# Optimization experiments

Measured on AMD Instinct MI355X. Metric: run time of the kernel, lower is better.

The kernel has to match this reference:

```python
import jax, jax.numpy as jnp
import numpy as np

B, M, T, D, V = 16, 4096, 4, 256, 40000
HOPS, NLAYER, CONV_MAX = 3, 3, 512
PAD = 1  # PAD_token: embedding row zeroed (padding_idx)


def setup_inputs() -> dict:
    key = jax.random.key(0)
    ks = jax.random.split(key, 10)
    story = jax.random.randint(ks[0], (B, M, T), 0, V)
    conv_len = jax.random.randint(ks[1], (B,), 1, CONV_MAX)
    kb_len = jax.random.randint(ks[2], (B,), 0, M - CONV_MAX)
    query = jax.random.normal(ks[3], (B, 1, D), jnp.float32)
    history_outputs = jax.random.normal(ks[4], (B, CONV_MAX, D), jnp.float32)
    query_vector = jax.random.normal(ks[5], (B, D), jnp.float32)
    global_pointer = jax.random.uniform(ks[6], (B, M), jnp.float32)
    # hop+1 embedding tables, N(0, 0.1), padding row zeroed
    C_emb = jax.random.normal(ks[7], (HOPS + 1, V, D), jnp.float32) * 0.1
    C_emb = C_emb.at[:, PAD, :].set(0.0)
    Tg_w = jax.random.normal(ks[8], (HOPS + 1, D, D), jnp.float32) * 0.05
    Tg_b = jnp.zeros((HOPS + 1, D), jnp.float32)
    FW_w = jax.random.normal(ks[9], (D, D), jnp.float32) * 0.05
    FW_b = jnp.zeros((D,), jnp.float32)
    return dict(story=story, kb_len=kb_len, conv_len=conv_len, query=query,
                history_outputs=history_outputs, query_vector=query_vector,
                global_pointer=global_pointer, C_emb=C_emb, Tg_w=Tg_w,
                Tg_b=Tg_b, FW_w=FW_w, FW_b=FW_b)


def _add_lm(mem, kb_len, conv_len, hist):
    # mem: [B,M,D]; add hist[b, 0:conv_len[b]] into mem[b, kb_len[b]:kb_len[b]+conv_len[b]]
    j = jnp.arange(mem.shape[1])[None, :]                       # [1,M]
    start = kb_len[:, None]
    mask = (j >= start) & (j < start + conv_len[:, None])       # [B,M]
    idx = jnp.clip(j - start, 0, hist.shape[1] - 1)             # [B,M]
    gathered = jnp.take_along_axis(hist, idx[..., None], axis=1)  # [B,M,D]
    return mem + jnp.where(mask[..., None], gathered, 0.0)


def _embed(table, story, kb_len, conv_len, hist):
    # bag-of-words over the mem-token axis, then LM-embedding add
    e = jnp.sum(table[story], axis=2)                           # [B,M,D]
    return _add_lm(e, kb_len, conv_len, hist)


def reference(story, kb_len, conv_len, query, history_outputs, query_vector,
              global_pointer, C_emb, Tg_w, Tg_b, FW_w, FW_b):
    # ---- load_memory (eval mode: dropout is identity; ablationH/G = False) ----
    q = query[:, 0, :]                                          # [B,D]
    last_u = None
    m_story = None
    for layer in range(NLAYER):
        iq = q
        if layer > 0:
            g = jax.nn.sigmoid(iq @ Tg_w[0].T + Tg_b[0])
            iq = last_u[0] * g + iq * (1.0 - g)
        u = [iq]
        m_story = []
        embC = None
        for hop in range(HOPS):
            embA = _embed(C_emb[hop], story, kb_len, conv_len, history_outputs)
            logit = jnp.einsum('bmd,bd->bm', embA, u[-1])
            prob = jax.nn.softmax(logit, axis=1)
            embC = _embed(C_emb[hop + 1], story, kb_len, conv_len, history_outputs)
            o_k = jnp.einsum('bm,bmd->bd', prob, embC)
            u_k = u[-1] + o_k
            if layer > 0:
                g = jax.nn.sigmoid(u_k @ Tg_w[hop + 1].T + Tg_b[hop + 1])
                u_k = last_u[hop + 1] * g + u_k * (1.0 - g)
            u.append(u_k)
            m_story.append(embA)
        m_story.append(embC)
        last_u = u
        q = jax.nn.relu(u[-1] @ FW_w.T + FW_b)
    # ---- forward (decoder-side read over last layer's memories) ----
    uf = query_vector
    psoft = None
    logits = None
    for hop in range(HOPS):
        mA = m_story[hop] * global_pointer[:, :, None]
        logits = jnp.einsum('bmd,bd->bm', mA, uf)
        psoft = jax.nn.softmax(logits, axis=1)
        mC = m_story[hop + 1] * global_pointer[:, :, None]
        uf = uf + jnp.einsum('bm,bmd->bd', psoft, mC)
    return (psoft, logits, uf, m_story[-1])
```

## Files before the change

### kernel.cpp

```cpp
#include <hip/hip_runtime.h>
#include <math.h>

#define Bdim 16
#define Mdim 4096
#define Tdim 4
#define Ddim 256
#define Vdim 40000
#define CONVMAX 512
#define MT 64

__global__ void init_kernel(const float* __restrict__ qv, float* __restrict__ uf) {
    int b = blockIdx.x, i = threadIdx.x;
    uf[(size_t)b * Ddim + i] = qv[(size_t)b * Ddim + i];
}

__global__ void qk_kernel(const int* __restrict__ story, const int* __restrict__ kb_len,
                          const int* __restrict__ conv_len, const float* __restrict__ hist,
                          const float* __restrict__ tab, const float* __restrict__ uf,
                          const float* __restrict__ gp, float* __restrict__ logits) {
    int tid = threadIdx.x, wave = tid >> 6, lane = tid & 63;
    int row0 = blockIdx.x * 16 + wave * 4;
    int b = row0 >> 12;
    int d4 = lane * 4;
    const float4 uv = *(const float4*)(uf + (size_t)b * Ddim + d4);
    int kb = kb_len[b], cl = conv_len[b];
#pragma unroll
    for (int r = 0; r < 4; ++r) {
        int row = row0 + r;
        int m = row & (Mdim - 1);
        const int* st = story + (size_t)row * Tdim;
        float4 acc = make_float4(0.f, 0.f, 0.f, 0.f);
#pragma unroll
        for (int t = 0; t < Tdim; ++t) {
            const float4 v = *(const float4*)(tab + (size_t)st[t] * Ddim + d4);
            acc.x += v.x; acc.y += v.y; acc.z += v.z; acc.w += v.w;
        }
        if (m >= kb && m < kb + cl) {
            const float4 h = *(const float4*)(hist + ((size_t)b * CONVMAX + (m - kb)) * Ddim + d4);
            acc.x += h.x; acc.y += h.y; acc.z += h.z; acc.w += h.w;
        }
        float p = acc.x * uv.x + acc.y * uv.y + acc.z * uv.z + acc.w * uv.w;
#pragma unroll
        for (int off = 32; off > 0; off >>= 1) p += __shfl_xor(p, off, 64);
        if (lane == 0) logits[row] = p * gp[row];
    }
}

__global__ void stats_kernel(const float* __restrict__ logits, float* __restrict__ maxv,
                             float* __restrict__ rsum) {
    int b = blockIdx.x, tid = threadIdx.x;
    __shared__ float sh[256];
    const float* lg = logits + (size_t)b * Mdim;
    float mx = -INFINITY;
    for (int i = tid; i < Mdim; i += 256) mx = fmaxf(mx, lg[i]);
    sh[tid] = mx; __syncthreads();
    for (int s = 128; s > 0; s >>= 1) { if (tid < s) sh[tid] = fmaxf(sh[tid], sh[tid + s]); __syncthreads(); }
    float bm = sh[0]; __syncthreads();
    float sm = 0.f;
    for (int i = tid; i < Mdim; i += 256) sm += expf(lg[i] - bm);
    sh[tid] = sm; __syncthreads();
    for (int s = 128; s > 0; s >>= 1) { if (tid < s) sh[tid] += sh[tid + s]; __syncthreads(); }
    if (tid == 0) { maxv[b] = bm; rsum[b] = 1.0f / sh[0]; }
}

__global__ void att_kernel(const int* __restrict__ story, const int* __restrict__ kb_len,
                           const int* __restrict__ conv_len, const float* __restrict__ hist,
                           const float* __restrict__ tab, const float* __restrict__ logits,
                           const float* __restrict__ maxv, const float* __restrict__ rsum,
                           const float* __restrict__ gp,
                           float* __restrict__ uf_acc, float* __restrict__ out_m,
                           float* __restrict__ out_psoft) {
    int bid = blockIdx.x;
    int b  = bid / (Mdim / MT);
    int m0 = (bid % (Mdim / MT)) * MT;
    int tid = threadIdx.x, wave = tid >> 6, lane = tid & 63;
    int d4 = lane * 4;
    __shared__ float prob[MT];
    __shared__ float4 red[4][64];
    if (tid < MT) {
        size_t row = (size_t)b * Mdim + m0 + tid;
        float pn = expf(logits[row] - maxv[b]) * rsum[b];
        if (out_psoft) out_psoft[row] = pn;
        prob[tid] = pn * gp[row];
    }
    __syncthreads();
    int kb = kb_len[b], cl = conv_len[b];
    float4 acc = make_float4(0.f, 0.f, 0.f, 0.f);
#pragma unroll 4
    for (int mm = wave; mm < MT; mm += 4) {
        int m = m0 + mm;
        size_t row = (size_t)b * Mdim + m;
        const int* st = story + row * Tdim;
        float4 v = make_float4(0.f, 0.f, 0.f, 0.f);
#pragma unroll
        for (int t = 0; t < Tdim; ++t) {
            const float4 w = *(const float4*)(tab + (size_t)st[t] * Ddim + d4);
            v.x += w.x; v.y += w.y; v.z += w.z; v.w += w.w;
        }
        if (m >= kb && m < kb + cl) {
            const float4 h = *(const float4*)(hist + ((size_t)b * CONVMAX + (m - kb)) * Ddim + d4);
            v.x += h.x; v.y += h.y; v.z += h.z; v.w += h.w;
        }
        if (out_m) *(float4*)(out_m + row * Ddim + d4) = v;
        float p = prob[mm];
        acc.x += p * v.x; acc.y += p * v.y; acc.z += p * v.z; acc.w += p * v.w;
    }
    red[wave][lane] = acc;
    __syncthreads();
    if (wave == 0) {
        float4 a0 = red[0][lane], a1 = red[1][lane], a2 = red[2][lane], a3 = red[3][lane];
        float* dst = uf_acc + (size_t)b * Ddim + d4;
        atomicAdd(dst + 0, a0.x + a1.x + a2.x + a3.x);
        atomicAdd(dst + 1, a0.y + a1.y + a2.y + a3.y);
        atomicAdd(dst + 2, a0.z + a1.z + a2.z + a3.z);
        atomicAdd(dst + 3, a0.w + a1.w + a2.w + a3.w);
    }
}

extern "C" void kernel_launch(void* const* d_in, const int* in_sizes, int n_in,
                              void* d_out, int out_size, void* d_ws, size_t ws_size,
                              hipStream_t stream) {
    const int*   story        = (const int*)d_in[0];
    const int*   kb_len       = (const int*)d_in[1];
    const int*   conv_len     = (const int*)d_in[2];
    const float* hist         = (const float*)d_in[4];
    const float* query_vector = (const float*)d_in[5];
    const float* gp           = (const float*)d_in[6];
    const float* C_emb        = (const float*)d_in[7];

    float* out        = (float*)d_out;
    float* out_psoft  = out;
    float* out_logits = out + (size_t)Bdim * Mdim;
    float* out_uf     = out + 2 * (size_t)Bdim * Mdim;
    float* out_m      = out + 2 * (size_t)Bdim * Mdim + (size_t)Bdim * Ddim;

    float* ws = (float*)d_ws;
    float* logits = ws;
    float* maxv   = logits + (size_t)Bdim * Mdim;
    float* rsum   = maxv + Bdim;

    const size_t TAB = (size_t)Vdim * Ddim;
    const float* tab0 = C_emb;
    const float* tab1 = C_emb + TAB;
    const float* tab2 = C_emb + 2 * TAB;
    const float* tab3 = C_emb + 3 * TAB;

    const int QK_GRID  = Bdim * Mdim / 16;
    const int ATT_GRID = Bdim * (Mdim / MT);

    init_kernel<<<Bdim, Ddim, 0, stream>>>(query_vector, out_uf);

    qk_kernel<<<QK_GRID, 256, 0, stream>>>(story, kb_len, conv_len, hist,
                                           tab0, query_vector, gp, logits);
    stats_kernel<<<Bdim, 256, 0, stream>>>(logits, maxv, rsum);
    att_kernel<<<ATT_GRID, 256, 0, stream>>>(story, kb_len, conv_len, hist,
                                             tab1, logits, maxv, rsum, gp,
                                             out_uf, nullptr, nullptr);
    qk_kernel<<<QK_GRID, 256, 0, stream>>>(story, kb_len, conv_len, hist,
                                           tab1, out_uf, gp, logits);
    stats_kernel<<<Bdim, 256, 0, stream>>>(logits, maxv, rsum);
    att_kernel<<<ATT_GRID, 256, 0, stream>>>(story, kb_len, conv_len, hist,
                                             tab2, logits, maxv, rsum, gp,
                                             out_uf, nullptr, nullptr);
    qk_kernel<<<QK_GRID, 256, 0, stream>>>(story, kb_len, conv_len, hist,
                                           tab2, out_uf, gp, out_logits);
    stats_kernel<<<Bdim, 256, 0, stream>>>(out_logits, maxv, rsum);
    att_kernel<<<ATT_GRID, 256, 0, stream>>>(story, kb_len, conv_len, hist,
                                             tab3, out_logits, maxv, rsum, gp,
                                             out_uf, out_m, out_psoft);
}
```

Measured before the change: 490.4 us.

## Reassociate hop reads over vocabulary: table-uf dot products and scattered weight sums

The logit computation is restructured to first dot every embedding-table row with all batch query vectors, giving a V×B table. Per-row logits then become four scalar lookups instead of gathering four 256-wide rows. The attention read is likewise reformulated: probabilities are scattered with atomics into per-vocab weights, and a dense pass over the table accumulates the output. This replaces random gathers of 64K rows × 4 tokens with streaming the 40000-row table, at the cost of atomic contention and extra launches. The final hop keeps the original kernel but uses nontemporal stores for the large memory output.

```diff
diff --git a/kernel.cpp b/kernel.cpp
--- a/kernel.cpp
+++ b/kernel.cpp
@@ -9,48 +9,80 @@
 #define CONVMAX 512
 #define MT 64
 
+typedef float f32x4 __attribute__((ext_vector_type(4)));
+static __device__ inline void nt_store4(float* p, float4 v) {
+    f32x4 x = {v.x, v.y, v.z, v.w};
+    __builtin_nontemporal_store(x, (f32x4*)p);
+}
+
 __global__ void init_kernel(const float* __restrict__ qv, float* __restrict__ uf) {
     int b = blockIdx.x, i = threadIdx.x;
     uf[(size_t)b * Ddim + i] = qv[(size_t)b * Ddim + i];
 }
 
-__global__ void qk_kernel(const int* __restrict__ story, const int* __restrict__ kb_len,
-                          const int* __restrict__ conv_len, const float* __restrict__ hist,
-                          const float* __restrict__ tab, const float* __restrict__ uf,
-                          const float* __restrict__ gp, float* __restrict__ logits) {
-    int tid = threadIdx.x, wave = tid >> 6, lane = tid & 63;
-    int row0 = blockIdx.x * 16 + wave * 4;
-    int b = row0 >> 12;
-    int d4 = lane * 4;
-    const float4 uv = *(const float4*)(uf + (size_t)b * Ddim + d4);
-    int kb = kb_len[b], cl = conv_len[b];
-#pragma unroll
-    for (int r = 0; r < 4; ++r) {
-        int row = row0 + r;
-        int m = row & (Mdim - 1);
-        const int* st = story + (size_t)row * Tdim;
-        float4 acc = make_float4(0.f, 0.f, 0.f, 0.f);
-#pragma unroll
-        for (int t = 0; t < Tdim; ++t) {
-            const float4 v = *(const float4*)(tab + (size_t)st[t] * Ddim + d4);
-            acc.x += v.x; acc.y += v.y; acc.z += v.z; acc.w += v.w;
-        }
-        if (m >= kb && m < kb + cl) {
-            const float4 h = *(const float4*)(hist + ((size_t)b * CONVMAX + (m - kb)) * Ddim + d4);
-            acc.x += h.x; acc.y += h.y; acc.z += h.z; acc.w += h.w;
-        }
-        float p = acc.x * uv.x + acc.y * uv.y + acc.z * uv.z + acc.w * uv.w;
-#pragma unroll
-        for (int off = 32; off > 0; off >>= 1) p += __shfl_xor(p, off, 64);
-        if (lane == 0) logits[row] = p * gp[row];
-    }
-}
-
-__global__ void stats_kernel(const float* __restrict__ logits, float* __restrict__ maxv,
-                             float* __restrict__ rsum) {
-    int b = blockIdx.x, tid = threadIdx.x;
+#define DV_VROWS 64
+#define DV_BLOCKS (Vdim / DV_VROWS)
+__global__ void dot_kernel(const float* __restrict__ tab, const float* __restrict__ uf,
+                           const float* __restrict__ hist,
+                           float* __restrict__ D, float* __restrict__ Hdot) {
+    __shared__ __align__(16) float ufs[Bdim * Ddim];
+    int tid = threadIdx.x;
+#pragma unroll
+    for (int k = 0; k < Bdim; ++k) ufs[k * Ddim + tid] = uf[k * Ddim + tid];
+    __syncthreads();
+    int wave = tid >> 6, lane = tid & 63;
+    int bid = blockIdx.x;
+    if (bid < DV_BLOCKS) {
+        int v0 = bid * DV_VROWS + wave * (DV_VROWS / 4);
+        for (int i = 0; i < DV_VROWS / 4; ++i) {
+            int v = v0 + i;
+            const float4 r = *(const float4*)(tab + (size_t)v * Ddim + lane * 4);
+#pragma unroll
+            for (int b = 0; b < Bdim; ++b) {
+                const float4 u4 = *(const float4*)(&ufs[b * Ddim + lane * 4]);
+                float s = r.x * u4.x + r.y * u4.y + r.z * u4.z + r.w * u4.w;
+#pragma unroll
+                for (int off = 32; off > 0; off >>= 1) s += __shfl_xor(s, off, 64);
+                if (lane == 0) D[v * Bdim + b] = s;
+            }
+        }
+    } else {
+        int b = bid - DV_BLOCKS;
+        for (int j = wave; j < CONVMAX; j += 4) {
+            const float4 r = *(const float4*)(hist + ((size_t)b * CONVMAX + j) * Ddim + lane * 4);
+            const float4 u4 = *(const float4*)(&ufs[b * Ddim + lane * 4]);
+            float s = r.x * u4.x + r.y * u4.y + r.z * u4.z + r.w * u4.w;
+#pragma unroll
+            for (int off = 32; off > 0; off >>= 1) s += __shfl_xor(s, off, 64);
+            if (lane == 0) Hdot[b * CONVMAX + j] = s;
+        }
+    }
+}
+
+__global__ void logit_kernel(const int* __restrict__ story, const int* __restrict__ kb_len,
+                             const int* __restrict__ conv_len, const float* __restrict__ D,
+                             const float* __restrict__ Hdot, const float* __restrict__ gp,
+                             float* __restrict__ logits) {
+    int row = blockIdx.x * 256 + threadIdx.x;
+    int b = row >> 12, m = row & (Mdim - 1);
+    const int4 st = *(const int4*)(story + (size_t)row * Tdim);
+    float l = D[st.x * Bdim + b] + D[st.y * Bdim + b] + D[st.z * Bdim + b] + D[st.w * Bdim + b];
+    unsigned j = (unsigned)(m - kb_len[b]);
+    if (j < (unsigned)conv_len[b]) l += Hdot[b * CONVMAX + j];
+    logits[row] = l * gp[row];
+}
+
+#define ZW_BLOCKS (Vdim * Bdim / 1024)
+__global__ void stats_zero_kernel(const float* __restrict__ logits, float* __restrict__ maxv,
+                                  float* __restrict__ rsum, float* __restrict__ w) {
+    int bid = blockIdx.x, tid = threadIdx.x;
+    if (bid >= Bdim) {
+        int idx = (bid - Bdim) * 1024 + tid * 4;
+        *(float4*)(w + idx) = make_float4(0.f, 0.f, 0.f, 0.f);
+        return;
+    }
     __shared__ float sh[256];
-    const float* lg = logits + (size_t)b * Mdim;
+    const float* lg = logits + (size_t)bid * Mdim;
     float mx = -INFINITY;
     for (int i = tid; i < Mdim; i += 256) mx = fmaxf(mx, lg[i]);
     sh[tid] = mx; __syncthreads();
@@ -60,7 +92,54 @@
     for (int i = tid; i < Mdim; i += 256) sm += expf(lg[i] - bm);
     sh[tid] = sm; __syncthreads();
     for (int s = 128; s > 0; s >>= 1) { if (tid < s) sh[tid] += sh[tid + s]; __syncthreads(); }
-    if (tid == 0) { maxv[b] = bm; rsum[b] = 1.0f / sh[0]; }
+    if (tid == 0) { maxv[bid] = bm; rsum[bid] = 1.0f / sh[0]; }
+}
+
+__global__ void scatter_kernel(const int* __restrict__ story, const int* __restrict__ kb_len,
+                               const int* __restrict__ conv_len, const float* __restrict__ logits,
+                               const float* __restrict__ maxv, const float* __restrict__ rsum,
+                               const float* __restrict__ gp, float* __restrict__ w,
+                               float* __restrict__ pwin) {
+    int row = blockIdx.x * 256 + threadIdx.x;
+    int b = row >> 12, m = row & (Mdim - 1);
+    float p = expf(logits[row] - maxv[b]) * rsum[b] * gp[row];
+    const int4 st = *(const int4*)(story + (size_t)row * Tdim);
+    atomicAdd(&w[st.x * Bdim + b], p);
+    atomicAdd(&w[st.y * Bdim + b], p);
+    atomicAdd(&w[st.z * Bdim + b], p);
+    atomicAdd(&w[st.w * Bdim + b], p);
+    unsigned j = (unsigned)(m - kb_len[b]);
+    if (j < (unsigned)conv_len[b]) pwin[b * CONVMAX + j] = p;
+}
+
+#define WS_VROWS 64
+#define WS_BLOCKS (Vdim / WS_VROWS)
+__global__ void wsum_kernel(const float* __restrict__ tab, const float* __restrict__ w,
+                            const float* __restrict__ pwin, const float* __restrict__ hist,
+                            const int* __restrict__ conv_len, float* __restrict__ uf) {
+    int tid = threadIdx.x, lane = tid & 63;
+    int bid = blockIdx.x;
+    if (bid < WS_BLOCKS) {
+        float acc[Bdim];
+#pragma unroll
+        for (int b = 0; b < Bdim; ++b) acc[b] = 0.f;
+        int v0 = bid * WS_VROWS;
+        for (int v = v0; v < v0 + WS_VROWS; ++v) {
+            float wv = (lane < Bdim) ? w[v * Bdim + lane] : 0.f;
+            float tv = tab[(size_t)v * Ddim + tid];
+#pragma unroll
+            for (int b = 0; b < Bdim; ++b) acc[b] += __shfl(wv, b, 64) * tv;
+        }
+#pragma unroll
+        for (int b = 0; b < Bdim; ++b) atomicAdd(&uf[b * Ddim + tid], acc[b]);
+    } else {
+        int b = bid - WS_BLOCKS;
+        int cl = conv_len[b];
+        float acc = 0.f;
+        for (int j = 0; j < cl; ++j)
+            acc += pwin[b * CONVMAX + j] * hist[((size_t)b * CONVMAX + j) * Ddim + tid];
+        atomicAdd(&uf[b * Ddim + tid], acc);
+    }
 }
 
 __global__ void att_kernel(const int* __restrict__ story, const int* __restrict__ kb_len,
@@ -80,7 +159,7 @@
     if (tid < MT) {
         size_t row = (size_t)b * Mdim + m0 + tid;
         float pn = expf(logits[row] - maxv[b]) * rsum[b];
-        if (out_psoft) out_psoft[row] = pn;
+        __builtin_nontemporal_store(pn, out_psoft + row);
         prob[tid] = pn * gp[row];
     }
     __syncthreads();
@@ -94,14 +173,14 @@
         float4 v = make_float4(0.f, 0.f, 0.f, 0.f);
 #pragma unroll
         for (int t = 0; t < Tdim; ++t) {
-            const float4 w = *(const float4*)(tab + (size_t)st[t] * Ddim + d4);
-            v.x += w.x; v.y += w.y; v.z += w.z; v.w += w.w;
+            const float4 wv = *(const float4*)(tab + (size_t)st[t] * Ddim + d4);
+            v.x += wv.x; v.y += wv.y; v.z += wv.z; v.w += wv.w;
         }
         if (m >= kb && m < kb + cl) {
             const float4 h = *(const float4*)(hist + ((size_t)b * CONVMAX + (m - kb)) * Ddim + d4);
             v.x += h.x; v.y += h.y; v.z += h.z; v.w += h.w;
         }
-        if (out_m) *(float4*)(out_m + row * Ddim + d4) = v;
+        nt_store4(out_m + row * Ddim + d4, v);
         float p = prob[mm];
         acc.x += p * v.x; acc.y += p * v.y; acc.z += p * v.z; acc.w += p * v.w;
     }
@@ -135,7 +214,11 @@
     float* out_m      = out + 2 * (size_t)Bdim * Mdim + (size_t)Bdim * Ddim;
 
     float* ws = (float*)d_ws;
-    float* logits = ws;
+    float* D      = ws;
+    float* w      = D + (size_t)Vdim * Bdim;
+    float* Hdot   = w + (size_t)Vdim * Bdim;
+    float* pwin   = Hdot + Bdim * CONVMAX;
+    float* logits = pwin + Bdim * CONVMAX;
     float* maxv   = logits + (size_t)Bdim * Mdim;
     float* rsum   = maxv + Bdim;
 
@@ -145,27 +228,29 @@
     const float* tab2 = C_emb + 2 * TAB;
     const float* tab3 = C_emb + 3 * TAB;
 
-    const int QK_GRID  = Bdim * Mdim / 16;
+    const int ROW_GRID = Bdim * Mdim / 256;
+    const int DOT_GRID = DV_BLOCKS + Bdim;
+    const int SZ_GRID  = Bdim + ZW_BLOCKS;
+    const int WS_GRID  = WS_BLOCKS + Bdim;
     const int ATT_GRID = Bdim * (Mdim / MT);
 
     init_kernel<<<Bdim, Ddim, 0, stream>>>(query_vector, out_uf);
 
-    qk_kernel<<<QK_GRID, 256, 0, stream>>>(story, kb_len, conv_len, hist,
-                                           tab0, query_vector, gp, logits);
-    stats_kernel<<<Bdim, 256, 0, stream>>>(logits, maxv, rsum);
-    att_kernel<<<ATT_GRID, 256, 0, stream>>>(story, kb_len, conv_len, hist,
-                                             tab1, logits, maxv, rsum, gp,
-                                             out_uf, nullptr, nullptr);
-    qk_kernel<<<QK_GRID, 256, 0, stream>>>(story, kb_len, conv_len, hist,
-                                           tab1, out_uf, gp, logits);
-    stats_kernel<<<Bdim, 256, 0, stream>>>(logits, maxv, rsum);
-    att_kernel<<<ATT_GRID, 256, 0, stream>>>(story, kb_len, conv_len, hist,
-                                             tab2, logits, maxv, rsum, gp,
-                                             out_uf, nullptr, nullptr);
-    qk_kernel<<<QK_GRID, 256, 0, stream>>>(story, kb_len, conv_len, hist,
-                                           tab2, out_uf, gp, out_logits);
-    stats_kernel<<<Bdim, 256, 0, stream>>>(out_logits, maxv, rsum);
-    att_kernel<<<ATT_GRID, 256, 0, stream>>>(story, kb_len, conv_len, hist,
-                                             tab3, out_logits, maxv, rsum, gp,
+    const float* qtab[3]  = { tab0, tab1, tab2 };
+    const float* vtab[3]  = { tab1, tab2, tab3 };
+    for (int h = 0; h < 2; ++h) {
+        dot_kernel<<<DOT_GRID, 256, 0, stream>>>(qtab[h], out_uf, hist, D, Hdot);
+        logit_kernel<<<ROW_GRID, 256, 0, stream>>>(story, kb_len, conv_len, D, Hdot, gp, logits);
+        stats_zero_kernel<<<SZ_GRID, 256, 0, stream>>>(logits, maxv, rsum, w);
+        scatter_kernel<<<ROW_GRID, 256, 0, stream>>>(story, kb_len, conv_len, logits,
+                                                     maxv, rsum, gp, w, pwin);
+        wsum_kernel<<<WS_GRID, 256, 0, stream>>>(vtab[h], w, pwin, hist, conv_len, out_uf);
+    }
+
+    dot_kernel<<<DOT_GRID, 256, 0, stream>>>(tab2, out_uf, hist, D, Hdot);
+    logit_kernel<<<ROW_GRID, 256, 0, stream>>>(story, kb_len, conv_len, D, Hdot, gp, out_logits);
+    stats_zero_kernel<<<SZ_GRID, 256, 0, stream>>>(out_logits, maxv, rsum, w);
+    att_kernel<<<ATT_GRID, 256, 0, stream>>>(story, kb_len, conv_len, hist, tab3,
+                                             out_logits, maxv, rsum, gp,
                                              out_uf, out_m, out_psoft);
 }
```

Measured after the change: 805.1 us. 1.64x slower.
